# Kernel optimization log

Hardware: AMD Instinct MI355X
Metric: run time of the kernel (lower is better)

The kernel has to match this reference:

```python
import jax, jax.numpy as jnp
import numpy as np

H, D = 16, 64  # heads, head dim; E = H*D


def setup_inputs() -> dict:
    key = jax.random.key(0)
    ks = jax.random.split(key, 8)
    B, T, E = 4, 1024, 1024
    s = (2.0 / E) ** 0.5
    return {
        "x": jax.random.normal(ks[0], (B, T, E), jnp.float32),
        "wq": jax.random.normal(ks[1], (H * D, E), jnp.float32) * s,
        "wk": jax.random.normal(ks[2], (H * D, E), jnp.float32) * s,
        "wv": jax.random.normal(ks[3], (H * D, E), jnp.float32) * s,
        "wvr": jax.random.normal(ks[4], (H * D, E), jnp.float32) * s,
        "wr": jax.random.normal(ks[5], (H, E, T), jnp.float32) * s,
        "wj": jax.random.normal(ks[6], (E, E), jnp.float32) * s,
        "gate": jnp.zeros((H, 3), jnp.float32),
        "wo": jax.random.normal(ks[7], (E, H * D), jnp.float32) * s,
    }


def reference(x, wq, wk, wv, wvr, wr, wj, gate, wo):
    B, T, E = x.shape
    scale = 1.0 / D ** 0.5

    def proj(w):  # torch Linear: y = x @ w.T, then split heads -> (B,H,T,D)
        return jnp.einsum('bte,fe->btf', x, w).reshape(B, T, H, D).transpose(0, 2, 1, 3)

    mask = jnp.triu(jnp.ones((T, T), bool), 1)  # True above diagonal (masked)

    # --- branch 1: standard causal QKV attention ---
    q, k, v = proj(wq), proj(wk), proj(wv)
    s1 = jnp.einsum('bhid,bhjd->bhij', q, k) * scale
    a1 = jax.nn.softmax(jnp.where(mask, -jnp.inf, s1), axis=-1)
    out1 = jnp.einsum('bhij,bhjd->bhid', a1, v)

    # --- branch 2: RRPRAM (parameter-based per-key scores, broadcast over queries) ---
    rv = proj(wvr)
    s2 = jnp.einsum('bte,het->bht', x, wr[:, :, :T]) * scale  # score per key position
    s2 = jnp.broadcast_to(s2[:, :, None, :], (B, H, T, T))
    a2 = jax.nn.softmax(jnp.where(mask, -jnp.inf, s2), axis=-1)
    out2 = jnp.einsum('bhij,bhjd->bhid', a2, rv)

    # --- branch 3: Janus self-echo (rank-1 outer-product scores) ---
    echo = jnp.einsum('bte,fe->btf', x, wj)            # x @ wj.T
    echo_back = jnp.einsum('btf,fe->bte', echo, wj)    # echo @ wj
    sc = jnp.sum(x * echo_back, axis=-1) / (E ** 0.5)  # (B,T)
    s3 = sc[:, :, None] * sc[:, None, :]               # (B,T,T)
    a3 = jax.nn.softmax(jnp.where(mask, -jnp.inf, s3), axis=-1)
    jv = echo.reshape(B, T, H, D).transpose(0, 2, 1, 3)
    out3 = jnp.einsum('bij,bhjd->bhid', a3, jv)

    # --- gated combine (softmax over the 3 branches per head) ---
    g = jax.nn.softmax(gate, axis=-1)  # (H,3)
    out = (g[:, 0][None, :, None, None] * out1
           + g[:, 1][None, :, None, None] * out2
           + g[:, 2][None, :, None, None] * out3)
    out = out.transpose(0, 2, 1, 3).reshape(B, T, H * D)
    return jnp.einsum('btf,ef->bte', out, wo)
```

## Files before the change

kernel.cpp:

```cpp
#include <hip/hip_runtime.h>
#include <cstdint>
#include <cstddef>

typedef unsigned short u16;
typedef short bf16x8 __attribute__((ext_vector_type(8)));
typedef short bf16x4 __attribute__((ext_vector_type(4)));
typedef float f32x4 __attribute__((ext_vector_type(4)));

constexpr int B_ = 4, T_ = 1024, E_ = 1024, H_ = 16, D_ = 64;

__device__ __forceinline__ float bf2f(u16 u) {
  union { unsigned u; float f; } v; v.u = ((unsigned)u) << 16; return v.f;
}
__device__ __forceinline__ u16 f2bf(float f) {
  union { float f; unsigned u; } v; v.f = f;
  return (u16)((v.u + 0x7fffu + ((v.u >> 16) & 1u)) >> 16);
}

#define GLD_LDS16(gp, lp)                                                      \
  __builtin_amdgcn_global_load_lds(                                            \
      (const __attribute__((address_space(1))) void*)(gp),                     \
      (__attribute__((address_space(3))) void*)(lp), 16, 0, 0)

#define SBAR()                                                                 \
  do {                                                                         \
    __builtin_amdgcn_sched_barrier(0);                                         \
    __builtin_amdgcn_s_barrier();                                              \
    __builtin_amdgcn_sched_barrier(0);                                         \
  } while (0)
#define WAIT_LGKM0()                                                           \
  do {                                                                         \
    asm volatile("s_waitcnt lgkmcnt(0)" ::: "memory");                         \
    __builtin_amdgcn_sched_barrier(0);                                         \
  } while (0)
#define WAIT_VM4()                                                             \
  do {                                                                         \
    asm volatile("s_waitcnt vmcnt(4)" ::: "memory");                           \
    __builtin_amdgcn_sched_barrier(0);                                         \
  } while (0)

__global__ __launch_bounds__(512, 2) void gemm_qkv8(
    const u16* __restrict__ A, const u16* __restrict__ Bm, u16* __restrict__ C)
{
  __shared__ u16 smem[65536];

  const int tid  = threadIdx.x;
  const int lane = tid & 63;
  const int wave = tid >> 6;
  const int wm = wave >> 2;
  const int wn = wave & 3;
  const int fr = lane & 15;
  const int fg = lane >> 4;
  const int fx = fr & 7;
  const int m0 = blockIdx.y * 256;
  const int n0 = blockIdx.x * 256;

  auto stage = [&](int ktl, int half) {
    const int buf = ktl & 1;
    int kt = (ktl > 15) ? 15 : ktl;
    const int k0 = kt << 6;
    const u16* src = (half < 2)
        ? (A  + (size_t)(m0 + (half & 1) * 128) * 1024)
        : (Bm + (size_t)(n0 + (half & 1) * 128) * 1024);
    u16* dst = smem + (buf << 15) + (half << 13);
    #pragma unroll
    for (int l = 0; l < 2; l++) {
      const int s = (l << 9) | tid;
      const int r = s >> 3, ch = s & 7;
      GLD_LDS16(src + (size_t)r * 1024 + k0 + ((ch ^ (r & 7)) << 3), dst + s * 8);
    }
  };

  f32x4 acc[8][4];
  #pragma unroll
  for (int i = 0; i < 8; i++)
    #pragma unroll
    for (int j = 0; j < 4; j++) acc[i][j] = f32x4{0.f, 0.f, 0.f, 0.f};

  stage(0, 0); stage(0, 1); stage(0, 2); stage(0, 3);
  stage(1, 2); stage(1, 0);
  WAIT_VM4();
  __builtin_amdgcn_s_barrier();
  __builtin_amdgcn_sched_barrier(0);

  const int ko0 = (fg ^ fx) << 3;
  const int ko1 = ((4 | fg) ^ fx) << 3;

  for (int t = 0; t < 16; t++) {
    const int buf = t & 1;
    const int ab = (buf << 15) + (wm << 13) + fr * 64;
    const int bb = (buf << 15) + 16384 + (wn << 12) + fr * 64;

    bf16x8 aF[4][2], bF[4][2];

    #pragma unroll
    for (int mt = 0; mt < 4; mt++) {
      aF[mt][0] = *(const bf16x8*)(smem + ab + mt * 1024 + ko0);
      aF[mt][1] = *(const bf16x8*)(smem + ab + mt * 1024 + ko1);
    }
    #pragma unroll
    for (int nt = 0; nt < 2; nt++) {
      bF[nt][0] = *(const bf16x8*)(smem + bb + nt * 1024 + ko0);
      bF[nt][1] = *(const bf16x8*)(smem + bb + nt * 1024 + ko1);
    }
    stage(t + 1, 1);
    SBAR();
    WAIT_LGKM0();
    __builtin_amdgcn_s_setprio(1);
    #pragma unroll
    for (int mt = 0; mt < 4; mt++)
      #pragma unroll
      for (int nt = 0; nt < 2; nt++) {
        acc[mt][nt] = __builtin_amdgcn_mfma_f32_16x16x32_bf16(aF[mt][0], bF[nt][0], acc[mt][nt], 0, 0, 0);
        acc[mt][nt] = __builtin_amdgcn_mfma_f32_16x16x32_bf16(aF[mt][1], bF[nt][1], acc[mt][nt], 0, 0, 0);
      }
    __builtin_amdgcn_s_setprio(0);
    SBAR();

    #pragma unroll
    for (int nt = 2; nt < 4; nt++) {
      bF[nt][0] = *(const bf16x8*)(smem + bb + nt * 1024 + ko0);
      bF[nt][1] = *(const bf16x8*)(smem + bb + nt * 1024 + ko1);
    }
    stage(t + 1, 3);
    SBAR();
    WAIT_LGKM0();
    __builtin_amdgcn_s_setprio(1);
    #pragma unroll
    for (int mt = 0; mt < 4; mt++)
      #pragma unroll
      for (int nt = 2; nt < 4; nt++) {
        acc[mt][nt] = __builtin_amdgcn_mfma_f32_16x16x32_bf16(aF[mt][0], bF[nt][0], acc[mt][nt], 0, 0, 0);
        acc[mt][nt] = __builtin_amdgcn_mfma_f32_16x16x32_bf16(aF[mt][1], bF[nt][1], acc[mt][nt], 0, 0, 0);
      }
    __builtin_amdgcn_s_setprio(0);
    SBAR();

    #pragma unroll
    for (int mt = 0; mt < 4; mt++) {
      aF[mt][0] = *(const bf16x8*)(smem + ab + (4 + mt) * 1024 + ko0);
      aF[mt][1] = *(const bf16x8*)(smem + ab + (4 + mt) * 1024 + ko1);
    }
    stage(t + 2, 2);
    SBAR();
    WAIT_LGKM0();
    __builtin_amdgcn_s_setprio(1);
    #pragma unroll
    for (int mt = 0; mt < 4; mt++)
      #pragma unroll
      for (int nt = 0; nt < 2; nt++) {
        acc[4 + mt][nt] = __builtin_amdgcn_mfma_f32_16x16x32_bf16(aF[mt][0], bF[nt][0], acc[4 + mt][nt], 0, 0, 0);
        acc[4 + mt][nt] = __builtin_amdgcn_mfma_f32_16x16x32_bf16(aF[mt][1], bF[nt][1], acc[4 + mt][nt], 0, 0, 0);
      }
    __builtin_amdgcn_s_setprio(0);
    SBAR();

    stage(t + 2, 0);
    SBAR();
    __builtin_amdgcn_s_setprio(1);
    #pragma unroll
    for (int mt = 0; mt < 4; mt++)
      #pragma unroll
      for (int nt = 2; nt < 4; nt++) {
        acc[4 + mt][nt] = __builtin_amdgcn_mfma_f32_16x16x32_bf16(aF[mt][0], bF[nt][0], acc[4 + mt][nt], 0, 0, 0);
        acc[4 + mt][nt] = __builtin_amdgcn_mfma_f32_16x16x32_bf16(aF[mt][1], bF[nt][1], acc[4 + mt][nt], 0, 0, 0);
      }
    __builtin_amdgcn_s_setprio(0);
    WAIT_VM4();
    __builtin_amdgcn_s_barrier();
    __builtin_amdgcn_sched_barrier(0);
  }

  u16* Cp = C + (size_t)(m0 + wm * 128) * 4096 + n0 + wn * 64;
  #pragma unroll
  for (int mt = 0; mt < 8; mt++)
    #pragma unroll
    for (int nt = 0; nt < 4; nt++)
      #pragma unroll
      for (int r2 = 0; r2 < 4; r2++)
        Cp[(size_t)(mt * 16 + fg * 4 + r2) * 4096 + nt * 16 + fr] = f2bf(acc[mt][nt][r2]);
}

template<int WM, int WN, int MT, int NT, bool CBF16>
__global__ __launch_bounds__(WM * WN * 64) void gemm_bt(
    const u16* __restrict__ A, const u16* __restrict__ Bm,
    void* __restrict__ Cv, int N, int K,
    int lda, int ldb, int ldc,
    long batchA, long batchB, long batchC, float alpha)
{
  constexpr int TM = WM * MT * 16;
  constexpr int TN = WN * NT * 16;
  constexpr int THREADS = WM * WN * 64;
  constexpr int ASZ = TM * 32, BSZ = TN * 32;

  __shared__ u16 smem[ASZ + BSZ];
  u16* sA = smem;
  u16* sB = smem + ASZ;

  const int z = blockIdx.z;
  const u16* Ab = A + (size_t)z * batchA;
  const u16* Bb = Bm + (size_t)z * batchB;
  const int m0 = blockIdx.y * TM;
  const int n0 = blockIdx.x * TN;
  const int tid = threadIdx.x;
  const int lane = tid & 63;
  const int wave = tid >> 6;
  const int wm = wave % WM;
  const int wn = wave / WM;
  const int fr = lane & 15;
  const int fg = lane >> 4;

  f32x4 acc[MT][NT];
  const f32x4 zero = {0.f, 0.f, 0.f, 0.f};
  #pragma unroll
  for (int i = 0; i < MT; i++)
    #pragma unroll
    for (int j = 0; j < NT; j++) acc[i][j] = zero;

  for (int k0 = 0; k0 < K; k0 += 32) {
    __syncthreads();
    for (int s = tid; s < TM * 4; s += THREADS) {
      const int row = s >> 2, ch = s & 3;
      GLD_LDS16(Ab + (size_t)(m0 + row) * lda + k0 + ch * 8, &sA[s * 8]);
    }
    for (int s = tid; s < TN * 4; s += THREADS) {
      const int row = s >> 2, ch = s & 3;
      int rr = n0 + row; if (rr > N - 1) rr = N - 1;
      GLD_LDS16(Bb + (size_t)rr * ldb + k0 + ch * 8, &sB[s * 8]);
    }
    __syncthreads();

    bf16x8 av[MT], bv[NT];
    #pragma unroll
    for (int mt = 0; mt < MT; mt++)
      av[mt] = *(const bf16x8*)&sA[((wm * MT + mt) * 16 + fr) * 32 + fg * 8];
    #pragma unroll
    for (int nt = 0; nt < NT; nt++)
      bv[nt] = *(const bf16x8*)&sB[((wn * NT + nt) * 16 + fr) * 32 + fg * 8];
    #pragma unroll
    for (int mt = 0; mt < MT; mt++)
      #pragma unroll
      for (int nt = 0; nt < NT; nt++)
        acc[mt][nt] = __builtin_amdgcn_mfma_f32_16x16x32_bf16(av[mt], bv[nt], acc[mt][nt], 0, 0, 0);
  }

  const int er = (lane >> 4) * 4;
  const int ec = lane & 15;
  #pragma unroll
  for (int mt = 0; mt < MT; mt++) {
    #pragma unroll
    for (int nt = 0; nt < NT; nt++) {
      const int row = m0 + (wm * MT + mt) * 16 + er;
      const int col = n0 + (wn * NT + nt) * 16 + ec;
      if (col < N) {
        #pragma unroll
        for (int r2 = 0; r2 < 4; r2++) {
          const float vv = acc[mt][nt][r2] * alpha;
          const size_t ci = (size_t)z * batchC + (size_t)(row + r2) * ldc + col;
          if constexpr (CBF16) ((u16*)Cv)[ci] = f2bf(vv);
          else                 ((float*)Cv)[ci] = vv;
        }
      }
    }
  }
}

__global__ __launch_bounds__(256) void gemm_echo(
    const u16* __restrict__ A, const u16* __restrict__ Alo,
    const u16* __restrict__ Bm, const u16* __restrict__ Blo,
    u16* __restrict__ echoT, float* __restrict__ sc)
{
  constexpr int TM = 128, TN = 64;
  constexpr int ASZ = TM * 32, BSZ = TN * 32;
  __shared__ u16 smem[2 * (ASZ + BSZ)];
  u16* sA  = smem;
  u16* sB  = smem + ASZ;
  u16* sAl = smem + ASZ + BSZ;
  u16* sBl = smem + 2 * ASZ + BSZ;

  const int m0 = blockIdx.y * TM;
  const int n0 = blockIdx.x * TN;
  const int tid = threadIdx.x;
  const int lane = tid & 63;
  const int wave = tid >> 6;
  const int wm = wave % 2;
  const int wn = wave / 2;
  const int fr = lane & 15, fg = lane >> 4;

  f32x4 acc[4][2];
  #pragma unroll
  for (int i = 0; i < 4; i++)
    #pragma unroll
    for (int j = 0; j < 2; j++) acc[i][j] = f32x4{0.f, 0.f, 0.f, 0.f};

  for (int k0 = 0; k0 < E_; k0 += 32) {
    __syncthreads();
    for (int s = tid; s < TM * 4; s += 256) {
      const int row = s >> 2, ch = s & 3;
      const size_t go = (size_t)(m0 + row) * E_ + k0 + ch * 8;
      GLD_LDS16(A + go, &sA[s * 8]);
      GLD_LDS16(Alo + go, &sAl[s * 8]);
    }
    for (int s = tid; s < TN * 4; s += 256) {
      const int row = s >> 2, ch = s & 3;
      const size_t go = (size_t)(n0 + row) * E_ + k0 + ch * 8;
      GLD_LDS16(Bm + go, &sB[s * 8]);
      GLD_LDS16(Blo + go, &sBl[s * 8]);
    }
    __syncthreads();

    bf16x8 av[4], bv[2], al[4], bl[2];
    #pragma unroll
    for (int mt = 0; mt < 4; mt++) {
      av[mt] = *(const bf16x8*)&sA[((wm * 4 + mt) * 16 + fr) * 32 + fg * 8];
      al[mt] = *(const bf16x8*)&sAl[((wm * 4 + mt) * 16 + fr) * 32 + fg * 8];
    }
    #pragma unroll
    for (int nt = 0; nt < 2; nt++) {
      bv[nt] = *(const bf16x8*)&sB[((wn * 2 + nt) * 16 + fr) * 32 + fg * 8];
      bl[nt] = *(const bf16x8*)&sBl[((wn * 2 + nt) * 16 + fr) * 32 + fg * 8];
    }
    #pragma unroll
    for (int mt = 0; mt < 4; mt++)
      #pragma unroll
      for (int nt = 0; nt < 2; nt++) {
        acc[mt][nt] = __builtin_amdgcn_mfma_f32_16x16x32_bf16(av[mt], bv[nt], acc[mt][nt], 0, 0, 0);
        acc[mt][nt] = __builtin_amdgcn_mfma_f32_16x16x32_bf16(al[mt], bv[nt], acc[mt][nt], 0, 0, 0);
        acc[mt][nt] = __builtin_amdgcn_mfma_f32_16x16x32_bf16(av[mt], bl[nt], acc[mt][nt], 0, 0, 0);
      }
  }

  __syncthreads();
  const int b   = m0 >> 10;
  const int t0l = m0 & 1023;
  const int ec  = lane & 15;
  u16* lt = smem;

  #pragma unroll
  for (int mt = 0; mt < 4; mt++) {
    float sq[4] = {0.f, 0.f, 0.f, 0.f};
    #pragma unroll
    for (int nt = 0; nt < 2; nt++) {
      const int cl = (wn * 2 + nt) * 16 + ec;
      #pragma unroll
      for (int r2 = 0; r2 < 4; r2++) {
        const float vv = acc[mt][nt][r2];
        sq[r2] += vv * vv;
        lt[cl * 132 + (wm * 4 + mt) * 16 + fg * 4 + r2] = f2bf(vv);
      }
    }
    #pragma unroll
    for (int m2 = 1; m2 < 16; m2 <<= 1) {
      sq[0] += __shfl_xor(sq[0], m2, 64);
      sq[1] += __shfl_xor(sq[1], m2, 64);
      sq[2] += __shfl_xor(sq[2], m2, 64);
      sq[3] += __shfl_xor(sq[3], m2, 64);
    }
    if (ec == 0) {
      #pragma unroll
      for (int r2 = 0; r2 < 4; r2++)
        atomicAdd(&sc[(size_t)b * T_ + t0l + (wm * 4 + mt) * 16 + fg * 4 + r2], sq[r2]);
    }
  }
  __syncthreads();
  for (int s = tid; s < 64 * 128; s += 256) {
    const int f = s >> 7, t = s & 127;
    echoT[((size_t)b * E_ + n0 + f) * T_ + t0l + t] = lt[f * 132 + t];
  }
}

__global__ __launch_bounds__(512, 2) void flash1p(
    const u16* __restrict__ qkvr, const u16* __restrict__ vTb, u16* __restrict__ out1) {
  const int x = blockIdx.x, h = blockIdx.y, b = blockIdx.z;
  const int tid = threadIdx.x, lane = tid & 63, w = tid >> 6;
  const int fr = lane & 15, fg = lane >> 4;
  const int itA = x, itB = 7 - x;

  __shared__ u16 sQ[8192];
  __shared__ u16 sK[2][8192];
  __shared__ u16 sV[2][8192];

  const u16* Kb = qkvr + (size_t)(b * T_) * 4096 + 1024 + h * 64;
  const u16* Vb = vTb + (size_t)(b * H_ + h) * (D_ * T_);

  auto stageQ = [&](int it) {
    const u16* Qb = qkvr + ((size_t)(b * T_) + it * 128) * 4096 + h * 64;
    #pragma unroll
    for (int s0 = 0; s0 < 1024; s0 += 512) {
      const int s = s0 + tid;
      const int l = s & 63, g = s >> 6;
      const int row = (g >> 1) * 16 + (l & 15);
      const int c8  = (g & 1) * 4 + (l >> 4);
      GLD_LDS16(Qb + (size_t)row * 4096 + c8 * 8, &sQ[s * 8]);
    }
  };
  auto stageKV = [&](int jt, int bi) {
    #pragma unroll
    for (int s0 = 0; s0 < 1024; s0 += 512) {
      const int s = s0 + tid;
      const int l = s & 63, g = s >> 6;
      const int row = (g >> 1) * 16 + (l & 15);
      const int c8  = (g & 1) * 4 + (l >> 4);
      GLD_LDS16(Kb + (size_t)(jt * 128 + row) * 4096 + c8 * 8, &sK[bi][s * 8]);
    }
    #pragma unroll
    for (int s0 = 0; s0 < 1024; s0 += 512) {
      const int s = s0 + tid;
      const int jc = s >> 6, d = s & 63;
      GLD_LDS16(Vb + ((size_t)(jt * 16 + jc)) * 512 + d * 8, &sV[bi][s * 8]);
    }
  };

  stageQ(itA);
  stageKV(0, 0);
  asm volatile("s_waitcnt vmcnt(0)" ::: "memory");
  __syncthreads();

  bf16x8 bQ[2];
  f32x4 accO[4];
  float mrow, lrow;

  #pragma unroll 1
  for (int ph = 0; ph < 2; ph++) {
    const int it    = ph ? itB : itA;
    const int sbase = ph ? (itA + 1) : 0;

    #pragma unroll
    for (int kk = 0; kk < 2; kk++)
      bQ[kk] = *(const bf16x8*)&sQ[((((w * 2) + kk) << 6) | lane) * 8];
    mrow = -3.0e38f; lrow = 0.f;
    #pragma unroll
    for (int nd = 0; nd < 4; nd++) accO[nd] = f32x4{0.f, 0.f, 0.f, 0.f};

    for (int jt = 0; jt <= it; jt++) {
      const int bi = (sbase + jt) & 1;

      if (jt < it) {
        stageKV(jt + 1, bi ^ 1);
      } else if (ph == 0) {
        stageQ(itB);
        stageKV(0, bi ^ 1);
      }

      f32x4 accST[8];
      #pragma unroll
      for (int nf = 0; nf < 8; nf++) accST[nf] = f32x4{0.f, 0.f, 0.f, 0.f};
      #pragma unroll
      for (int kk = 0; kk < 2; kk++) {
        #pragma unroll
        for (int nf = 0; nf < 8; nf++) {
          const bf16x8 aK = *(const bf16x8*)&sK[bi][((((nf << 1) | kk) << 6) | lane) * 8];
          accST[nf] = __builtin_amdgcn_mfma_f32_16x16x32_bf16(aK, bQ[kk], accST[nf], 0, 0, 0);
        }
      }

      const bool diag = (jt == it);
      const int iloc = w * 16 + fr;
      float sv[8][4];
      float rmax = -3.0e38f;
      #pragma unroll
      for (int nf = 0; nf < 8; nf++)
        #pragma unroll
        for (int r = 0; r < 4; r++) {
          float s = accST[nf][r] * 0.125f;
          if (diag && (nf * 16 + fg * 4 + r) > iloc) s = -3.0e38f;
          sv[nf][r] = s;
          rmax = fmaxf(rmax, s);
        }
      rmax = fmaxf(rmax, __shfl_xor(rmax, 16, 64));
      rmax = fmaxf(rmax, __shfl_xor(rmax, 32, 64));
      const float mn = fmaxf(mrow, rmax);
      const float al = __expf(mrow - mn);
      mrow = mn;
      float ps = 0.f;
      bf16x4 pf[8];
      #pragma unroll
      for (int nf = 0; nf < 8; nf++)
        #pragma unroll
        for (int r = 0; r < 4; r++) {
          const float pv = __expf(sv[nf][r] - mn);
          ps += pv;
          pf[nf][r] = (short)f2bf(pv);
        }
      ps += __shfl_xor(ps, 16, 64);
      ps += __shfl_xor(ps, 32, 64);
      lrow = lrow * al + ps;
      #pragma unroll
      for (int r = 0; r < 4; r++) {
        const float alr = __shfl(al, fg * 4 + r, 64);
        #pragma unroll
        for (int nd = 0; nd < 4; nd++) accO[nd][r] *= alr;
      }

      #pragma unroll
      for (int kc = 0; kc < 8; kc++) {
        bf16x8 bV[4];
        #pragma unroll
        for (int nd = 0; nd < 4; nd++) {
          const bf16x4 vv = *(const bf16x4*)&sV[bi][
              (((kc * 2 + (fg >> 1)) * 64 + nd * 16 + fr) * 8) + (fg & 1) * 4];
          bV[nd] = bf16x8{vv[0], vv[1], vv[2], vv[3], 0, 0, 0, 0};
        }
        const bf16x4 pp = pf[kc];
        const bf16x8 pA = bf16x8{pp[0], pp[1], pp[2], pp[3], 0, 0, 0, 0};
        #pragma unroll
        for (int nd = 0; nd < 4; nd++)
          accO[nd] = __builtin_amdgcn_mfma_f32_16x16x32_bf16(pA, bV[nd], accO[nd], 0, 0, 0);
      }

      asm volatile("s_waitcnt vmcnt(0)" ::: "memory");
      __syncthreads();
    }

    u16* op = out1 + ((size_t)(b * T_) + it * 128) * E_ + h * 64;
    const float li = 1.0f / lrow;
    #pragma unroll
    for (int r = 0; r < 4; r++) {
      const float linv = __shfl(li, fg * 4 + r, 64);
      const int row = w * 16 + fg * 4 + r;
      #pragma unroll
      for (int nd = 0; nd < 4; nd++)
        op[(size_t)row * E_ + nd * 16 + fr] = f2bf(accO[nd][r] * linv);
    }
  }
}

__device__ __forceinline__ float block_max256(float v, float* red) {
  #pragma unroll
  for (int m = 32; m > 0; m >>= 1) v = fmaxf(v, __shfl_xor(v, m, 64));
  if ((threadIdx.x & 63) == 0) red[threadIdx.x >> 6] = v;
  __syncthreads();
  const float r = fmaxf(fmaxf(red[0], red[1]), fmaxf(red[2], red[3]));
  __syncthreads();
  return r;
}
__device__ __forceinline__ float block_sum256(float v, float* red) {
  #pragma unroll
  for (int m = 32; m > 0; m >>= 1) v += __shfl_xor(v, m, 64);
  if ((threadIdx.x & 63) == 0) red[threadIdx.x >> 6] = v;
  __syncthreads();
  const float r = (red[0] + red[1]) + (red[2] + red[3]);
  __syncthreads();
  return r;
}

__global__ __launch_bounds__(256) void cast_all(
    const float* __restrict__ x, const float* __restrict__ wq,
    const float* __restrict__ wk, const float* __restrict__ wv,
    const float* __restrict__ wvr, const float* __restrict__ wo,
    const float* __restrict__ wj,
    u16* __restrict__ xb, u16* __restrict__ xlo, u16* __restrict__ wcat,
    u16* __restrict__ wob, u16* __restrict__ wjb, u16* __restrict__ wjlo) {
  const int bid = blockIdx.x;
  if (bid < 4096) {
    const size_t i = ((size_t)bid * 256 + threadIdx.x) * 4;
    const float4 v = *(const float4*)(x + i);
    ushort4 oh, ol;
    oh.x = f2bf(v.x); ol.x = f2bf(v.x - bf2f(oh.x));
    oh.y = f2bf(v.y); ol.y = f2bf(v.y - bf2f(oh.y));
    oh.z = f2bf(v.z); ol.z = f2bf(v.z - bf2f(oh.z));
    oh.w = f2bf(v.w); ol.w = f2bf(v.w - bf2f(oh.w));
    *(ushort4*)(xb + i) = oh;
    *(ushort4*)(xlo + i) = ol;
  } else if (bid < 8192) {
    const int r = (bid - 4096) >> 10;
    const float* src = (r == 0) ? wq : (r == 1) ? wk : (r == 2) ? wv : wvr;
    const size_t i = ((size_t)((bid - 4096) & 1023) * 256 + threadIdx.x) * 4;
    const float4 v = *(const float4*)(src + i);
    ushort4 o;
    o.x = f2bf(v.x); o.y = f2bf(v.y); o.z = f2bf(v.z); o.w = f2bf(v.w);
    *(ushort4*)(wcat + (size_t)r * (1 << 20) + i) = o;
  } else if (bid < 9216) {
    const size_t i = ((size_t)(bid - 8192) * 256 + threadIdx.x) * 4;
    const float4 v = *(const float4*)(wo + i);
    ushort4 o;
    o.x = f2bf(v.x); o.y = f2bf(v.y); o.z = f2bf(v.z); o.w = f2bf(v.w);
    *(ushort4*)(wob + i) = o;
  } else {
    const size_t i = ((size_t)(bid - 9216) * 256 + threadIdx.x) * 4;
    const float4 v = *(const float4*)(wj + i);
    ushort4 oh, ol;
    oh.x = f2bf(v.x); ol.x = f2bf(v.x - bf2f(oh.x));
    oh.y = f2bf(v.y); ol.y = f2bf(v.y - bf2f(oh.y));
    oh.z = f2bf(v.z); ol.z = f2bf(v.z - bf2f(oh.z));
    oh.w = f2bf(v.w); ol.w = f2bf(v.w - bf2f(oh.w));
    *(ushort4*)(wjb + i) = oh;
    *(ushort4*)(wjlo + i) = ol;
  }
}

__global__ __launch_bounds__(256) void s2_direct(
    const u16* __restrict__ xb, const float* __restrict__ wr, float* __restrict__ s2) {
  const int t0 = blockIdx.x * 32, h = blockIdx.y;
  const int tt = threadIdx.x & 31, eg = threadIdx.x >> 5;
  float acc[4] = {0.f, 0.f, 0.f, 0.f};
  const float* wp = wr + (size_t)h * E_ * T_ + t0 + tt;
  for (int ec = 0; ec < 8; ec++) {
    const int e0 = ec * 128 + eg * 16;
    bf16x8 xv[4][2];
    #pragma unroll
    for (int b = 0; b < 4; b++) {
      const u16* xp = xb + ((size_t)(b * T_) + t0 + tt) * E_ + e0;
      xv[b][0] = *(const bf16x8*)xp;
      xv[b][1] = *(const bf16x8*)(xp + 8);
    }
    #pragma unroll
    for (int e2 = 0; e2 < 16; e2++) {
      const float w = wp[(size_t)(e0 + e2) * T_];
      #pragma unroll
      for (int b = 0; b < 4; b++)
        acc[b] += bf2f((u16)xv[b][e2 >> 3][e2 & 7]) * w;
    }
  }
  __shared__ float red[8][4][33];
  #pragma unroll
  for (int b = 0; b < 4; b++) red[eg][b][tt] = acc[b];
  __syncthreads();
  if (threadIdx.x < 128) {
    const int b = threadIdx.x >> 5, t = threadIdx.x & 31;
    float s = 0.f;
    #pragma unroll
    for (int g = 0; g < 8; g++) s += red[g][b][t];
    s2[((size_t)b * H_ + h) * T_ + t0 + t] = s * 0.125f;
  }
}

__global__ __launch_bounds__(256) void a3_softmax(const float* __restrict__ sc, u16* __restrict__ a3) {
  const int i = blockIdx.x;
  const int b = blockIdx.y;
  const float* sr = sc + (size_t)b * T_;
  const float sci = sr[i] * 0.03125f;
  u16* row = a3 + ((size_t)b * T_ + i) * T_;
  __shared__ float red[4];
  float v[4];
  float m = -3.0e38f;
  #pragma unroll
  for (int k = 0; k < 4; k++) {
    const int j = threadIdx.x + k * 256;
    const float xv = (j <= i) ? sci * (sr[j] * 0.03125f) : -3.0e38f;
    v[k] = xv;
    m = fmaxf(m, xv);
  }
  m = block_max256(m, red);
  float s = 0.f;
  #pragma unroll
  for (int k = 0; k < 4; k++) {
    const int j = threadIdx.x + k * 256;
    const float p = (j <= i) ? __expf(v[k] - m) : 0.f;
    v[k] = p;
    s += p;
  }
  s = block_sum256(s, red);
  const float inv = 1.0f / s;
  #pragma unroll
  for (int k = 0; k < 4; k++) {
    const int j = threadIdx.x + k * 256;
    row[j] = f2bf(v[k] * inv);
  }
}

__global__ __launch_bounds__(1024) void branch2_scan(
    const float* __restrict__ s2, const u16* __restrict__ rv, int ldrv,
    u16* __restrict__ out2) {
  const int h = blockIdx.x, b = blockIdx.y;
  const int tid = threadIdx.x;
  const int lane = tid & 63;
  const int wv = tid >> 6;

  const float* srow = s2 + ((size_t)b * H_ + h) * T_;

  __shared__ float wbuf[T_];
  __shared__ float numtot[16][64];
  __shared__ float dentot[16];
  __shared__ float redm[16];

  float m = srow[tid];
  #pragma unroll
  for (int mk = 32; mk > 0; mk >>= 1) m = fmaxf(m, __shfl_xor(m, mk, 64));
  if (lane == 0) redm[wv] = m;
  __syncthreads();
  m = redm[0];
  #pragma unroll
  for (int i2 = 1; i2 < 16; i2++) m = fmaxf(m, redm[i2]);

  wbuf[tid] = __expf(srow[tid] - m);
  __syncthreads();

  const u16* rvp = rv + (size_t)(b * T_) * ldrv + h * D_ + lane;
  const int j0 = wv * 64;
  float num = 0.f, den = 0.f;
  #pragma unroll 8
  for (int j2 = 0; j2 < 64; j2++) {
    const float w = wbuf[j0 + j2];
    den += w;
    num += w * bf2f(rvp[(size_t)(j0 + j2) * ldrv]);
  }
  numtot[wv][lane] = num;
  if (lane == 0) dentot[wv] = den;
  __syncthreads();

  float num_off = 0.f, den_off = 0.f;
  for (int w2 = 0; w2 < wv; w2++) {
    num_off += numtot[w2][lane];
    den_off += dentot[w2];
  }

  u16* op = out2 + (size_t)b * T_ * E_ + h * D_ + lane;
  num = num_off; den = den_off;
  #pragma unroll 8
  for (int j2 = 0; j2 < 64; j2++) {
    const float w = wbuf[j0 + j2];
    num += w * bf2f(rvp[(size_t)(j0 + j2) * ldrv]);
    den += w;
    op[(size_t)(j0 + j2) * E_] = f2bf(num / den);
  }
}

__global__ __launch_bounds__(256) void transpose_v(const u16* __restrict__ v, u16* __restrict__ vTb,
                                                   int ldv) {
  const int bh = blockIdx.x;
  const int b = bh >> 4, h = bh & 15;
  const int d0 = blockIdx.y * 32, t0 = blockIdx.z * 32;
  __shared__ u16 tile[32][33];
  const int c = threadIdx.x & 31, r0 = threadIdx.x >> 5;
  #pragma unroll
  for (int rr = 0; rr < 32; rr += 8) {
    const int t = t0 + rr + r0;
    tile[rr + r0][c] = v[((size_t)b * T_ + t) * ldv + h * 64 + d0 + c];
  }
  __syncthreads();
  #pragma unroll
  for (int rr = 0; rr < 32; rr += 8) {
    const int d = d0 + rr + r0;
    const int t = t0 + c;
    vTb[((size_t)(bh * 128 + (t >> 3)) * 64 + d) * 8 + (t & 7)] = tile[c][rr + r0];
  }
}

__global__ __launch_bounds__(256) void combine_gate(
    const u16* __restrict__ o1, const u16* __restrict__ o2, const u16* __restrict__ o3,
    const float* __restrict__ gate, u16* __restrict__ comb) {
  const size_t idx = (size_t)blockIdx.x * 256 + threadIdx.x;
  const int f = (int)(idx & (E_ - 1));
  const int h = f >> 6;
  const float g0 = gate[h * 3 + 0], g1 = gate[h * 3 + 1], g2 = gate[h * 3 + 2];
  const float mx = fmaxf(g0, fmaxf(g1, g2));
  const float e0 = __expf(g0 - mx), e1 = __expf(g1 - mx), e2 = __expf(g2 - mx);
  const float inv = 1.0f / (e0 + e1 + e2);
  const float o = (e0 * bf2f(o1[idx]) + e1 * bf2f(o2[idx]) + e2 * bf2f(o3[idx])) * inv;
  comb[idx] = f2bf(o);
}

extern "C" void kernel_launch(void* const* d_in, const int* in_sizes, int n_in,
                              void* d_out, int out_size, void* d_ws, size_t ws_size,
                              hipStream_t stream) {
  (void)in_sizes; (void)n_in; (void)out_size; (void)ws_size;
  const float* x    = (const float*)d_in[0];
  const float* wq   = (const float*)d_in[1];
  const float* wk   = (const float*)d_in[2];
  const float* wv   = (const float*)d_in[3];
  const float* wvr  = (const float*)d_in[4];
  const float* wr   = (const float*)d_in[5];
  const float* wj   = (const float*)d_in[6];
  const float* gate = (const float*)d_in[7];
  const float* wo   = (const float*)d_in[8];
  float* out = (float*)d_out;

  char* p = (char*)d_ws;
  auto alloc = [&](size_t bytes) -> char* {
    char* r = p; p += (bytes + 255) & ~(size_t)255; return r;
  };
  const size_t NTE = (size_t)B_ * T_ * E_;
  const size_t NW  = (size_t)E_ * E_;

  u16* xb    = (u16*)alloc(NTE * 2);
  u16* xlo   = (u16*)alloc(NTE * 2);
  u16* wcat  = (u16*)alloc(4 * NW * 2);
  u16* wjb   = (u16*)alloc(NW * 2);
  u16* wjlo  = (u16*)alloc(NW * 2);
  u16* wob   = (u16*)alloc(NW * 2);
  u16* qkvr  = (u16*)alloc(NTE * 4 * 2);
  u16* vT    = (u16*)alloc(NTE * 2);
  u16* echoT = (u16*)alloc(NTE * 2);
  u16* a3p   = (u16*)alloc(NTE * 2);
  float* sc  = (float*)alloc((size_t)B_ * T_ * 4);
  float* s2  = (float*)alloc((size_t)B_ * H_ * T_ * 4);
  u16* out1b = (u16*)alloc(NTE * 2);
  u16* out2b = (u16*)alloc(NTE * 2);
  u16* out3b = (u16*)alloc(NTE * 2);
  u16* comb  = (u16*)alloc(NTE * 2);

  cast_all<<<dim3(10240), 256, 0, stream>>>(x, wq, wk, wv, wvr, wo, wj,
                                            xb, xlo, wcat, wob, wjb, wjlo);
  hipMemsetAsync(sc, 0, (size_t)B_ * T_ * 4, stream);

  gemm_qkv8<<<dim3(16, 16), 512, 0, stream>>>(xb, wcat, qkvr);

  gemm_echo<<<dim3(16, 32, 1), 256, 0, stream>>>(xb, xlo, wjb, wjlo, echoT, sc);

  transpose_v<<<dim3(B_ * H_, D_ / 32, T_ / 32), 256, 0, stream>>>(qkvr + 2048, vT, 4096);
  s2_direct<<<dim3(T_ / 32, H_), 256, 0, stream>>>(xb, wr, s2);

  branch2_scan<<<dim3(H_, B_), 1024, 0, stream>>>(s2, qkvr + 3072, 4096, out2b);

  a3_softmax<<<dim3(T_, B_), 256, 0, stream>>>(sc, a3p);
  gemm_bt<2,2,4,2,true><<<dim3(E_ / 64, T_ / 128, B_), 256, 0, stream>>>(
      a3p, echoT, out3b, E_, T_, T_, T_, E_,
      (long)T_ * T_, (long)E_ * T_, (long)T_ * E_, 1.f);

  flash1p<<<dim3(4, H_, B_), 512, 0, stream>>>(qkvr, vT, out1b);

  combine_gate<<<dim3((unsigned)(NTE / 256)), 256, 0, stream>>>(out1b, out2b, out3b, gate, comb);
  gemm_bt<2,2,4,2,false><<<dim3(E_ / 64, (B_ * T_) / 128, 1), 256, 0, stream>>>(
      comb, wob, out, E_, E_, E_, E_, E_, 0L, 0L, 0L, 1.f);
}
```

Baseline: 361.5 us.

## Rewrite echo GEMM as 8-wave 128x128 tile with double-buffered swizzled LDS pipeline

```diff
diff --git a/kernel.cpp b/kernel.cpp
--- a/kernel.cpp
+++ b/kernel.cpp
@@ -265,27 +265,40 @@
   }
 }
 
-__global__ __launch_bounds__(256) void gemm_echo(
+__global__ __launch_bounds__(512, 2) void gemm_echo8(
     const u16* __restrict__ A, const u16* __restrict__ Alo,
     const u16* __restrict__ Bm, const u16* __restrict__ Blo,
     u16* __restrict__ echoT, float* __restrict__ sc)
 {
-  constexpr int TM = 128, TN = 64;
-  constexpr int ASZ = TM * 32, BSZ = TN * 32;
-  __shared__ u16 smem[2 * (ASZ + BSZ)];
-  u16* sA  = smem;
-  u16* sB  = smem + ASZ;
-  u16* sAl = smem + ASZ + BSZ;
-  u16* sBl = smem + 2 * ASZ + BSZ;
-
-  const int m0 = blockIdx.y * TM;
-  const int n0 = blockIdx.x * TN;
-  const int tid = threadIdx.x;
+  __shared__ u16 smem[65536];
+
+  const int tid  = threadIdx.x;
   const int lane = tid & 63;
   const int wave = tid >> 6;
-  const int wm = wave % 2;
-  const int wn = wave / 2;
-  const int fr = lane & 15, fg = lane >> 4;
+  const int wm = wave >> 2;
+  const int wn = wave & 3;
+  const int fr = lane & 15;
+  const int fg = lane >> 4;
+  const int fx = fr & 7;
+  const int m0 = blockIdx.y * 128;
+  const int n0 = blockIdx.x * 128;
+
+  auto stage = [&](int ktl, int unit) {
+    const int buf = ktl & 1;
+    int kt = (ktl > 15) ? 15 : ktl;
+    const int k0 = kt << 6;
+    const u16* src = (unit == 0) ? A   + (size_t)m0 * 1024
+                   : (unit == 1) ? Alo + (size_t)m0 * 1024
+                   : (unit == 2) ? Bm  + (size_t)n0 * 1024
+                   :               Blo + (size_t)n0 * 1024;
+    u16* dst = smem + (buf << 15) + (unit << 13);
+    #pragma unroll
+    for (int l = 0; l < 2; l++) {
+      const int s = (l << 9) | tid;
+      const int r = s >> 3, ch = s & 7;
+      GLD_LDS16(src + (size_t)r * 1024 + k0 + ((ch ^ (r & 7)) << 3), dst + s * 8);
+    }
+  };
 
   f32x4 acc[4][2];
   #pragma unroll
@@ -293,47 +306,99 @@
     #pragma unroll
     for (int j = 0; j < 2; j++) acc[i][j] = f32x4{0.f, 0.f, 0.f, 0.f};
 
-  for (int k0 = 0; k0 < E_; k0 += 32) {
-    __syncthreads();
-    for (int s = tid; s < TM * 4; s += 256) {
-      const int row = s >> 2, ch = s & 3;
-      const size_t go = (size_t)(m0 + row) * E_ + k0 + ch * 8;
-      GLD_LDS16(A + go, &sA[s * 8]);
-      GLD_LDS16(Alo + go, &sAl[s * 8]);
-    }
-    for (int s = tid; s < TN * 4; s += 256) {
-      const int row = s >> 2, ch = s & 3;
-      const size_t go = (size_t)(n0 + row) * E_ + k0 + ch * 8;
-      GLD_LDS16(Bm + go, &sB[s * 8]);
-      GLD_LDS16(Blo + go, &sBl[s * 8]);
-    }
-    __syncthreads();
-
-    bf16x8 av[4], bv[2], al[4], bl[2];
+  stage(0, 0); stage(0, 1); stage(0, 2); stage(0, 3);
+  stage(1, 0); stage(1, 1);
+  WAIT_VM4();
+  __builtin_amdgcn_s_barrier();
+  __builtin_amdgcn_sched_barrier(0);
+
+  const int ko0 = (fg ^ fx) << 3;
+  const int ko1 = ((4 | fg) ^ fx) << 3;
+
+  for (int t = 0; t < 16; t++) {
+    const int buf = t & 1;
+    const int ab = (buf << 15) + (wm * 64 + fr) * 64;
+    const int bb = (buf << 15) + 16384 + (wn * 32 + fr) * 64;
+
+    bf16x8 aH[4][2], aL[4][2], bH, bL;
+
     #pragma unroll
     for (int mt = 0; mt < 4; mt++) {
-      av[mt] = *(const bf16x8*)&sA[((wm * 4 + mt) * 16 + fr) * 32 + fg * 8];
-      al[mt] = *(const bf16x8*)&sAl[((wm * 4 + mt) * 16 + fr) * 32 + fg * 8];
-    }
-    #pragma unroll
-    for (int nt = 0; nt < 2; nt++) {
-      bv[nt] = *(const bf16x8*)&sB[((wn * 2 + nt) * 16 + fr) * 32 + fg * 8];
-      bl[nt] = *(const bf16x8*)&sBl[((wn * 2 + nt) * 16 + fr) * 32 + fg * 8];
-    }
-    #pragma unroll
-    for (int mt = 0; mt < 4; mt++)
-      #pragma unroll
-      for (int nt = 0; nt < 2; nt++) {
-        acc[mt][nt] = __builtin_amdgcn_mfma_f32_16x16x32_bf16(av[mt], bv[nt], acc[mt][nt], 0, 0, 0);
-        acc[mt][nt] = __builtin_amdgcn_mfma_f32_16x16x32_bf16(al[mt], bv[nt], acc[mt][nt], 0, 0, 0);
-        acc[mt][nt] = __builtin_amdgcn_mfma_f32_16x16x32_bf16(av[mt], bl[nt], acc[mt][nt], 0, 0, 0);
-      }
-  }
-
-  __syncthreads();
+      aH[mt][0] = *(const bf16x8*)(smem + ab + mt * 1024 + ko0);
+      aH[mt][1] = *(const bf16x8*)(smem + ab + mt * 1024 + ko1);
+      aL[mt][0] = *(const bf16x8*)(smem + ab + 8192 + mt * 1024 + ko0);
+      aL[mt][1] = *(const bf16x8*)(smem + ab + 8192 + mt * 1024 + ko1);
+    }
+    bH = *(const bf16x8*)(smem + bb + ko0);
+    bL = *(const bf16x8*)(smem + bb + 8192 + ko0);
+    stage(t + 1, 2);
+    SBAR();
+    WAIT_LGKM0();
+    __builtin_amdgcn_s_setprio(1);
+    #pragma unroll
+    for (int mt = 0; mt < 4; mt++) {
+      acc[mt][0] = __builtin_amdgcn_mfma_f32_16x16x32_bf16(aH[mt][0], bH, acc[mt][0], 0, 0, 0);
+      acc[mt][0] = __builtin_amdgcn_mfma_f32_16x16x32_bf16(aL[mt][0], bH, acc[mt][0], 0, 0, 0);
+      acc[mt][0] = __builtin_amdgcn_mfma_f32_16x16x32_bf16(aH[mt][0], bL, acc[mt][0], 0, 0, 0);
+    }
+    __builtin_amdgcn_s_setprio(0);
+    SBAR();
+
+    bH = *(const bf16x8*)(smem + bb + ko1);
+    bL = *(const bf16x8*)(smem + bb + 8192 + ko1);
+    stage(t + 1, 3);
+    SBAR();
+    WAIT_LGKM0();
+    __builtin_amdgcn_s_setprio(1);
+    #pragma unroll
+    for (int mt = 0; mt < 4; mt++) {
+      acc[mt][0] = __builtin_amdgcn_mfma_f32_16x16x32_bf16(aH[mt][1], bH, acc[mt][0], 0, 0, 0);
+      acc[mt][0] = __builtin_amdgcn_mfma_f32_16x16x32_bf16(aL[mt][1], bH, acc[mt][0], 0, 0, 0);
+      acc[mt][0] = __builtin_amdgcn_mfma_f32_16x16x32_bf16(aH[mt][1], bL, acc[mt][0], 0, 0, 0);
+    }
+    __builtin_amdgcn_s_setprio(0);
+    SBAR();
+
+    bH = *(const bf16x8*)(smem + bb + 1024 + ko0);
+    bL = *(const bf16x8*)(smem + bb + 8192 + 1024 + ko0);
+    stage(t + 2, 0);
+    SBAR();
+    WAIT_LGKM0();
+    __builtin_amdgcn_s_setprio(1);
+    #pragma unroll
+    for (int mt = 0; mt < 4; mt++) {
+      acc[mt][1] = __builtin_amdgcn_mfma_f32_16x16x32_bf16(aH[mt][0], bH, acc[mt][1], 0, 0, 0);
+      acc[mt][1] = __builtin_amdgcn_mfma_f32_16x16x32_bf16(aL[mt][0], bH, acc[mt][1], 0, 0, 0);
+      acc[mt][1] = __builtin_amdgcn_mfma_f32_16x16x32_bf16(aH[mt][0], bL, acc[mt][1], 0, 0, 0);
+    }
+    __builtin_amdgcn_s_setprio(0);
+    SBAR();
+
+    bH = *(const bf16x8*)(smem + bb + 1024 + ko1);
+    bL = *(const bf16x8*)(smem + bb + 8192 + 1024 + ko1);
+    stage(t + 2, 1);
+    SBAR();
+    WAIT_LGKM0();
+    __builtin_amdgcn_s_setprio(1);
+    #pragma unroll
+    for (int mt = 0; mt < 4; mt++) {
+      acc[mt][1] = __builtin_amdgcn_mfma_f32_16x16x32_bf16(aH[mt][1], bH, acc[mt][1], 0, 0, 0);
+      acc[mt][1] = __builtin_amdgcn_mfma_f32_16x16x32_bf16(aL[mt][1], bH, acc[mt][1], 0, 0, 0);
+      acc[mt][1] = __builtin_amdgcn_mfma_f32_16x16x32_bf16(aH[mt][1], bL, acc[mt][1], 0, 0, 0);
+    }
+    __builtin_amdgcn_s_setprio(0);
+    WAIT_VM4();
+    __builtin_amdgcn_s_barrier();
+    __builtin_amdgcn_sched_barrier(0);
+  }
+
+  asm volatile("s_waitcnt vmcnt(0) lgkmcnt(0)" ::: "memory");
+  __builtin_amdgcn_sched_barrier(0);
+  __builtin_amdgcn_s_barrier();
+  __builtin_amdgcn_sched_barrier(0);
+
   const int b   = m0 >> 10;
   const int t0l = m0 & 1023;
-  const int ec  = lane & 15;
   u16* lt = smem;
 
   #pragma unroll
@@ -341,12 +406,12 @@
     float sq[4] = {0.f, 0.f, 0.f, 0.f};
     #pragma unroll
     for (int nt = 0; nt < 2; nt++) {
-      const int cl = (wn * 2 + nt) * 16 + ec;
+      const int cl = wn * 32 + nt * 16 + fr;
       #pragma unroll
       for (int r2 = 0; r2 < 4; r2++) {
         const float vv = acc[mt][nt][r2];
         sq[r2] += vv * vv;
-        lt[cl * 132 + (wm * 4 + mt) * 16 + fg * 4 + r2] = f2bf(vv);
+        lt[cl * 132 + wm * 64 + mt * 16 + fg * 4 + r2] = f2bf(vv);
       }
     }
     #pragma unroll
@@ -356,16 +421,16 @@
       sq[2] += __shfl_xor(sq[2], m2, 64);
       sq[3] += __shfl_xor(sq[3], m2, 64);
     }
-    if (ec == 0) {
+    if (fr == 0) {
       #pragma unroll
       for (int r2 = 0; r2 < 4; r2++)
-        atomicAdd(&sc[(size_t)b * T_ + t0l + (wm * 4 + mt) * 16 + fg * 4 + r2], sq[r2]);
-    }
-  }
-  __syncthreads();
-  for (int s = tid; s < 64 * 128; s += 256) {
-    const int f = s >> 7, t = s & 127;
-    echoT[((size_t)b * E_ + n0 + f) * T_ + t0l + t] = lt[f * 132 + t];
+        atomicAdd(&sc[(size_t)b * T_ + t0l + wm * 64 + mt * 16 + fg * 4 + r2], sq[r2]);
+    }
+  }
+  __syncthreads();
+  for (int s = tid; s < 128 * 128; s += 512) {
+    const int f = s >> 7, tt = s & 127;
+    echoT[((size_t)b * E_ + n0 + f) * T_ + t0l + tt] = lt[f * 132 + tt];
   }
 }
 
@@ -796,7 +861,7 @@
 
   gemm_qkv8<<<dim3(16, 16), 512, 0, stream>>>(xb, wcat, qkvr);
 
-  gemm_echo<<<dim3(16, 32, 1), 256, 0, stream>>>(xb, xlo, wjb, wjlo, echoT, sc);
+  gemm_echo8<<<dim3(8, 32), 512, 0, stream>>>(xb, xlo, wjb, wjlo, echoT, sc);
 
   transpose_v<<<dim3(B_ * H_, D_ / 32, T_ / 32), 256, 0, stream>>>(qkvr + 2048, vT, 4096);
   s2_direct<<<dim3(T_ / 32, H_), 256, 0, stream>>>(xb, wr, s2);
```

After: 352.9 us. 1.02x faster.
